# Kernel optimization log

Hardware: AMD Instinct MI355X
Metric: run time of the kernel (lower is better)

The kernel has to match this reference:

```python
import jax, jax.numpy as jnp
import numpy as np

L, D, H, KS, VS, HID = 2048, 1024, 16, 1024, 1024, 4096
EPS = 1e-5


def _linear_params(key, din, dout):
    # torch nn.Linear default init: U(-1/sqrt(din), 1/sqrt(din))
    s = 1.0 / np.sqrt(din)
    kw, kb = jax.random.split(key)
    W = jax.random.uniform(kw, (dout, din), minval=-s, maxval=s, dtype=jnp.float32)
    b = jax.random.uniform(kb, (dout,), minval=-s, maxval=s, dtype=jnp.float32)
    return W, b


def setup_inputs() -> dict:
    key = jax.random.key(0)
    ks = jax.random.split(key, 12)
    x = jax.random.normal(ks[0], (L, D), dtype=jnp.float32)
    # inverse shortest-path lengths in [0, 1]
    shortest_path = jax.random.uniform(ks[1], (L, L), dtype=jnp.float32)
    Wq, bq = _linear_params(ks[2], D, KS)
    Wk, bk = _linear_params(ks[3], D, KS)
    Wv, bv = _linear_params(ks[4], D, VS)
    Wqp, bqp = _linear_params(ks[5], KS, KS)
    Wkp, bkp = _linear_params(ks[6], KS, KS)
    Wvp, bvp = _linear_params(ks[7], VS, VS)
    Wo, bo = _linear_params(ks[8], VS, D)
    W1, b1 = _linear_params(ks[9], D, HID)
    W2, b2 = _linear_params(ks[10], HID, D)
    g1 = jnp.ones((D,), jnp.float32); be1 = jnp.zeros((D,), jnp.float32)
    g2 = jnp.ones((D,), jnp.float32); be2 = jnp.zeros((D,), jnp.float32)
    return dict(x=x, shortest_path=shortest_path,
                Wq=Wq, bq=bq, Wk=Wk, bk=bk, Wv=Wv, bv=bv,
                Wqp=Wqp, bqp=bqp, Wkp=Wkp, bkp=bkp, Wvp=Wvp, bvp=bvp,
                Wo=Wo, bo=bo, W1=W1, b1=b1, W2=W2, b2=b2,
                g1=g1, be1=be1, g2=g2, be2=be2)


def _dense(h, W, b):
    return h @ W.T + b


def _layernorm(h, g, b):
    mu = jnp.mean(h, axis=-1, keepdims=True)
    var = jnp.mean(jnp.square(h - mu), axis=-1, keepdims=True)
    return (h - mu) * jax.lax.rsqrt(var + EPS) * g + b


def reference(x, shortest_path, Wq, bq, Wk, bk, Wv, bv, Wqp, bqp, Wkp, bkp,
              Wvp, bvp, Wo, bo, W1, b1, W2, b2, g1, be1, g2, be2):
    hd = KS // H
    vhd = VS // H
    q = _dense(_dense(x, Wq, bq), Wqp, bqp).reshape(L, H, hd).transpose(1, 0, 2)   # [H,L,hd]
    k = _dense(_dense(x, Wk, bk), Wkp, bkp).reshape(L, H, hd).transpose(1, 0, 2)   # [H,L,hd]
    v = _dense(_dense(x, Wv, bv), Wvp, bvp).reshape(L, H, vhd).transpose(1, 0, 2)  # [H,L,vhd]
    att = jnp.einsum('hld,hmd->hlm', q, k) / jnp.sqrt(jnp.float32(hd))             # [H,L,L]
    sp_bias = jax.nn.softmax(shortest_path, axis=-1) * 0.5                          # [L,L]
    att = jax.nn.softmax(att + sp_bias[None, :, :], axis=-1)
    o = jnp.einsum('hlm,hmd->hld', att, v).transpose(1, 0, 2).reshape(L, VS)        # [L,VS]
    o = _dense(o, Wo, bo)
    h = _layernorm(x + o, g1, be1)                # residual + LN1 (dropout=identity)
    f = jax.nn.relu(_dense(jax.nn.relu(_dense(h, W1, b1)), W2, b2))
    return _layernorm(h + f, g2, be2)             # residual + LN2
```

## Files before the change

kernel.cpp:

```cpp
#include <hip/hip_runtime.h>

typedef __attribute__((ext_vector_type(4))) float f32x4;
typedef __attribute__((ext_vector_type(8))) short s16x8;

static __device__ __forceinline__ ushort f2b(float f) {
  union { float f; unsigned u; } v; v.f = f;
  unsigned u = v.u;
  unsigned r = (u + 0x7fffu + ((u >> 16) & 1u)) >> 16;
  return (ushort)r;
}
static __device__ __forceinline__ float b2f(ushort h) {
  union { unsigned u; float f; } v; v.u = ((unsigned)h) << 16;
  return v.f;
}
static __device__ __forceinline__ unsigned cvtpk(float a, float b) {
  unsigned r;
  asm("v_cvt_pk_bf16_f32 %0, %1, %2" : "=v"(r) : "v"(a), "v"(b));
  return r;
}

static __device__ __forceinline__ void gload_lds16(const ushort* g, ushort* l) {
  __builtin_amdgcn_global_load_lds(
      (const __attribute__((address_space(1))) void*)g,
      (__attribute__((address_space(3))) void*)l, 16, 0, 0);
}

struct Cvt7 {
  const float* src[7];
  ushort* dst[7];
  int n[7];
};
__global__ __launch_bounds__(256) void cvt_multi_k(Cvt7 a) {
  int e = blockIdx.y;
  int i = (blockIdx.x * 256 + threadIdx.x) * 4;
  if (i >= a.n[e]) return;
  float4 v4 = *(const float4*)(a.src[e] + i);
  ushort4 o4; o4.x = f2b(v4.x); o4.y = f2b(v4.y); o4.z = f2b(v4.z); o4.w = f2b(v4.w);
  *(ushort4*)(a.dst[e] + i) = o4;
}

__global__ __launch_bounds__(256) void wtr_k(const float* __restrict__ Wq,
                                             const float* __restrict__ Wk,
                                             const float* __restrict__ Wv,
                                             ushort* __restrict__ dst) {
  __shared__ float t[64][65];
  int z = blockIdx.z;
  const float* src = z == 0 ? Wq : (z == 1 ? Wk : Wv);
  float scale = z == 0 ? 0.125f : 1.f;
  int r0 = blockIdx.x * 64, c0 = blockIdx.y * 64;
  int lr = threadIdx.x >> 2, lc4 = (threadIdx.x & 3) * 16;
#pragma unroll
  for (int j = 0; j < 4; ++j)
    *(float4*)&t[lr][lc4 + j * 4] = *(const float4*)(src + (size_t)(r0 + lr) * 1024 + c0 + lc4 + j * 4);
  __syncthreads();
  ushort tmp[16];
#pragma unroll
  for (int j = 0; j < 16; ++j) tmp[j] = f2b(t[lc4 + j][lr] * scale);
  ushort* d = dst + (size_t)z * 1048576 + (size_t)(c0 + lr) * 1024 + r0 + lc4;
  *(uint4*)d = *(uint4*)tmp;
  *(uint4*)(d + 8) = *(uint4*)(tmp + 8);
}

__global__ __launch_bounds__(256) void bvec_k(
    const float* __restrict__ Wqp, const float* __restrict__ Wkp, const float* __restrict__ Wvp,
    const float* __restrict__ bq, const float* __restrict__ bqp,
    const float* __restrict__ bk, const float* __restrict__ bkp,
    const float* __restrict__ bv, const float* __restrict__ bvp,
    float* __restrict__ outb) {
  int r = blockIdx.x * 4 + (threadIdx.x >> 6);
  int lane = threadIdx.x & 63;
  int z = r >> 10, rr = r & 1023;
  const float* Wp = z == 0 ? Wqp : (z == 1 ? Wkp : Wvp);
  const float* bi = z == 0 ? bq : (z == 1 ? bk : bv);
  const float* bp = z == 0 ? bqp : (z == 1 ? bkp : bvp);
  float s = 0.f;
#pragma unroll
  for (int t = 0; t < 4; ++t) {
    float4 w = *(const float4*)(Wp + (size_t)rr * 1024 + lane * 16 + t * 4);
    float4 b = *(const float4*)(bi + lane * 16 + t * 4);
    s += w.x * b.x + w.y * b.y + w.z * b.z + w.w * b.w;
  }
#pragma unroll
  for (int m = 1; m < 64; m <<= 1) s += __shfl_xor(s, m);
  if (lane == 0) outb[r] = (s + bp[rr]) * (z == 0 ? 0.125f : 1.f);
}

__global__ __launch_bounds__(256) void spsm_k(const float* __restrict__ sp,
                                              ushort* __restrict__ out) {
  const int Lc = 2048;
  int row = blockIdx.x;
  int tid = threadIdx.x;
  const float* r = sp + (size_t)row * Lc;
  float v[8];
  float mx = -1e30f;
#pragma unroll
  for (int j = 0; j < 8; ++j) { v[j] = r[tid + j * 256]; mx = fmaxf(mx, v[j]); }
#pragma unroll
  for (int m = 1; m < 64; m <<= 1) mx = fmaxf(mx, __shfl_xor(mx, m));
  __shared__ float redm[4], reds[4];
  if ((tid & 63) == 0) redm[tid >> 6] = mx;
  __syncthreads();
  mx = fmaxf(fmaxf(redm[0], redm[1]), fmaxf(redm[2], redm[3]));
  float s = 0.f;
#pragma unroll
  for (int j = 0; j < 8; ++j) { v[j] = __expf(v[j] - mx); s += v[j]; }
#pragma unroll
  for (int m = 1; m < 64; m <<= 1) s += __shfl_xor(s, m);
  if ((tid & 63) == 0) reds[tid >> 6] = s;
  __syncthreads();
  s = reds[0] + reds[1] + reds[2] + reds[3];
  float inv = 0.5f / s;
  ushort* o = out + (size_t)row * Lc;
#pragma unroll
  for (int j = 0; j < 8; ++j) o[tid + j * 256] = f2b(v[j] * inv);
}

__global__ __launch_bounds__(256) void vtr_k(const ushort* __restrict__ qkv,
                                             ushort* __restrict__ vT) {
  __shared__ ushort t[64][72];
  int tid = threadIdx.x;
  int r = tid >> 3, c8 = (tid & 7) * 8;
  int l0 = blockIdx.x * 64, h = blockIdx.y;
#pragma unroll
  for (int p = 0; p < 2; ++p)
    *(uint4*)&t[r + p * 32][c8] =
        *(const uint4*)(qkv + (size_t)(l0 + r + p * 32) * 3072 + 2048 + h * 64 + c8);
  __syncthreads();
#pragma unroll
  for (int p = 0; p < 2; ++p) {
    int d = r + p * 32;
    ushort tmp[8];
#pragma unroll
    for (int j = 0; j < 8; ++j) tmp[j] = t[c8 + j][d];
    *(uint4*)(vT + ((size_t)h * 64 + d) * 2048 + l0 + c8) = *(uint4*)tmp;
  }
}

template <int BM, int ZM>
__global__ __launch_bounds__(256, 2) void gemm_k(
    const ushort* __restrict__ A, const ushort* __restrict__ W,
    const float* __restrict__ bias, void* __restrict__ Cv,
    int M, int N, int K, int relu, float oscale) {
  constexpr int MT = BM / 32;
  __shared__ ushort As0[BM][64], Bs0[128][64];
  __shared__ ushort As1[BM][64], Bs1[128][64];
  const int z = (ZM != 0) ? blockIdx.z : 0;
  if (ZM == 1) { A += (size_t)z * M * K; W += (size_t)z * N * K; }
  int kb0 = 0, kb1 = K;
  if (ZM == 2) { int kh = K >> 1; kb0 = z * kh; kb1 = kb0 + kh; }
  const int tid = threadIdx.x;
  const int lane = tid & 63;
  const int wave = tid >> 6;
  const int wm = (wave >> 1) * (BM / 2);
  const int wn = (wave & 1) * 64;
  const int bm = blockIdx.x * BM;
  const int bn = blockIdx.y * 128;
  const int cl = lane & 15, rg = lane >> 4;
  const int lrow = lane >> 3, lcol = (lane & 7) * 8;

  f32x4 acc[MT][4];
#pragma unroll
  for (int i = 0; i < MT; ++i)
#pragma unroll
    for (int j = 0; j < 4; ++j) acc[i][j] = (f32x4){0.f, 0.f, 0.f, 0.f};

  const ushort* gA = A + (size_t)(bm + wave * 8 + lrow) * K + lcol;
  const ushort* gB = W + (size_t)(bn + wave * 8 + lrow) * K + lcol;

  auto stage = [&](ushort* lA, ushort* lB, int k0) {
#pragma unroll
    for (int c = 0; c < MT; ++c)
      gload_lds16(gA + (size_t)(c * 32) * K + k0, lA + wave * 512 + c * 2048);
#pragma unroll
    for (int c = 0; c < 4; ++c)
      gload_lds16(gB + (size_t)(c * 32) * K + k0, lB + wave * 512 + c * 2048);
  };
  auto compute = [&](const ushort* As, const ushort* Bs) {
    const int kbo = 8 * rg;
#pragma unroll
    for (int kk = 0; kk < 64; kk += 32) {
      s16x8 af[MT], bf[4];
#pragma unroll
      for (int mt = 0; mt < MT; ++mt)
        af[mt] = *(const s16x8*)(As + (wm + mt * 16 + cl) * 64 + kk + kbo);
#pragma unroll
      for (int nt = 0; nt < 4; ++nt)
        bf[nt] = *(const s16x8*)(Bs + (wn + nt * 16 + cl) * 64 + kk + kbo);
#pragma unroll
      for (int mt = 0; mt < MT; ++mt)
#pragma unroll
        for (int nt = 0; nt < 4; ++nt)
          acc[mt][nt] = __builtin_amdgcn_mfma_f32_16x16x32_bf16(af[mt], bf[nt], acc[mt][nt], 0, 0, 0);
    }
  };

  const int ktiles = (kb1 - kb0) >> 6;
  stage(&As0[0][0], &Bs0[0][0], kb0);
  __syncthreads();
  for (int tt = 0; tt < ktiles; tt += 2) {
    stage(&As1[0][0], &Bs1[0][0], kb0 + (tt + 1) * 64);
    compute(&As0[0][0], &Bs0[0][0]);
    __syncthreads();
    if (tt + 2 < ktiles) stage(&As0[0][0], &Bs0[0][0], kb0 + (tt + 2) * 64);
    compute(&As1[0][0], &Bs1[0][0]);
    __syncthreads();
  }

  if (ZM == 2) {
    float* Cf = (float*)Cv + (size_t)z * M * N;
#pragma unroll
    for (int nt = 0; nt < 4; ++nt) {
      int c = bn + wn + nt * 16 + cl;
#pragma unroll
      for (int mt = 0; mt < MT; ++mt)
#pragma unroll
        for (int i = 0; i < 4; ++i) {
          int r = bm + wm + mt * 16 + rg * 4 + i;
          Cf[(size_t)r * N + c] = acc[mt][nt][i];
        }
    }
  } else {
    ushort* Cu = (ushort*)Cv;
    if (ZM == 1) Cu += (size_t)z * M * N;
#pragma unroll
    for (int nt = 0; nt < 4; ++nt) {
      int c = bn + wn + nt * 16 + cl;
      float bv = bias ? bias[c] : 0.f;
#pragma unroll
      for (int mt = 0; mt < MT; ++mt) {
        float v0 = (acc[mt][nt][0] + bv) * oscale;
        float v1 = (acc[mt][nt][1] + bv) * oscale;
        float v2 = (acc[mt][nt][2] + bv) * oscale;
        float v3 = (acc[mt][nt][3] + bv) * oscale;
        if (relu) {
          v0 = fmaxf(v0, 0.f); v1 = fmaxf(v1, 0.f);
          v2 = fmaxf(v2, 0.f); v3 = fmaxf(v3, 0.f);
        }
        unsigned p01 = cvtpk(v0, v1), p23 = cvtpk(v2, v3);
        size_t b = (size_t)(bm + wm + mt * 16 + rg * 4) * N + c;
        Cu[b] = (ushort)p01;
        Cu[b + N] = (ushort)(p01 >> 16);
        Cu[b + 2 * N] = (ushort)p23;
        Cu[b + 3 * N] = (ushort)(p23 >> 16);
      }
    }
  }
}

__global__ __launch_bounds__(256, 2) void attn_k(
    const ushort* __restrict__ qkv, const ushort* __restrict__ vT,
    const ushort* __restrict__ biasb, ushort* __restrict__ opart,
    float* __restrict__ lbuf) {
  const int Lc = 2048;
  int h = blockIdx.x;
  int m0 = blockIdx.y * 64;
  int s = blockIdx.z;
  int nb = s * 1024, ne = nb + 1024;
  int tid = threadIdx.x, lane = tid & 63, wave = tid >> 6;

  __shared__ ushort Ks[64][72];
  __shared__ ushort Vs[64][72];
  __shared__ ushort Ps[4][16][72];
  __shared__ ushort Bs2[64][72];

  const int rg = lane >> 4, cl = lane & 15;
  const int kb = 8 * rg;
  int srow = tid >> 3, scol = (tid & 7) * 8;

  const ushort* qp = qkv + (size_t)(m0 + wave * 16 + cl) * 3072 + h * 64;
  s16x8 qfr[2];
  qfr[0] = *(const s16x8*)(qp + kb);
  qfr[1] = *(const s16x8*)(qp + 32 + kb);

  f32x4 oacc[4];
#pragma unroll
  for (int i = 0; i < 4; ++i) oacc[i] = (f32x4){0.f, 0.f, 0.f, 0.f};
  float lacc[4] = {0.f, 0.f, 0.f, 0.f};

  for (int n0 = nb; n0 < ne; n0 += 64) {
    __syncthreads();
#pragma unroll
    for (int pp = 0; pp < 2; ++pp) {
      int r = srow + pp * 32;
      *(uint4*)&Ks[r][scol] = *(const uint4*)(qkv + (size_t)(n0 + r) * 3072 + 1024 + h * 64 + scol);
      *(uint4*)&Vs[r][scol] = *(const uint4*)(vT + ((size_t)h * 64 + r) * 2048 + n0 + scol);
      *(uint4*)&Bs2[r][scol] = *(const uint4*)(biasb + (size_t)(m0 + r) * Lc + n0 + scol);
    }
    __syncthreads();

    f32x4 sacc[4];
#pragma unroll
    for (int nt = 0; nt < 4; ++nt)
#pragma unroll
      for (int i = 0; i < 4; ++i)
        sacc[nt][i] = b2f(Bs2[wave * 16 + rg * 4 + i][nt * 16 + cl]) - 8.f;

    __builtin_amdgcn_s_setprio(1);
#pragma unroll
    for (int kk2 = 0; kk2 < 2; ++kk2) {
#pragma unroll
      for (int nt = 0; nt < 4; ++nt) {
        s16x8 b = *(const s16x8*)&Ks[nt * 16 + cl][kk2 * 32 + kb];
        sacc[nt] = __builtin_amdgcn_mfma_f32_16x16x32_bf16(qfr[kk2], b, sacc[nt], 0, 0, 0);
      }
    }
    __builtin_amdgcn_s_setprio(0);

#pragma unroll
    for (int i = 0; i < 4; ++i) {
#pragma unroll
      for (int nt = 0; nt < 4; ++nt) {
        float pv = __expf(sacc[nt][i]);
        sacc[nt][i] = pv;
        lacc[i] += pv;
      }
    }
#pragma unroll
    for (int nt = 0; nt < 4; ++nt) {
      unsigned p01 = cvtpk(sacc[nt][0], sacc[nt][1]);
      unsigned p23 = cvtpk(sacc[nt][2], sacc[nt][3]);
      Ps[wave][rg * 4 + 0][nt * 16 + cl] = (ushort)p01;
      Ps[wave][rg * 4 + 1][nt * 16 + cl] = (ushort)(p01 >> 16);
      Ps[wave][rg * 4 + 2][nt * 16 + cl] = (ushort)p23;
      Ps[wave][rg * 4 + 3][nt * 16 + cl] = (ushort)(p23 >> 16);
    }
    __builtin_amdgcn_s_setprio(1);
#pragma unroll
    for (int kk = 0; kk < 64; kk += 32) {
      s16x8 a = *(const s16x8*)&Ps[wave][cl][kk + kb];
#pragma unroll
      for (int nt = 0; nt < 4; ++nt) {
        s16x8 b = *(const s16x8*)&Vs[nt * 16 + cl][kk + kb];
        oacc[nt] = __builtin_amdgcn_mfma_f32_16x16x32_bf16(a, b, oacc[nt], 0, 0, 0);
      }
    }
    __builtin_amdgcn_s_setprio(0);
  }
#pragma unroll
  for (int nt = 0; nt < 4; ++nt) {
    unsigned p01 = cvtpk(oacc[nt][0], oacc[nt][1]);
    unsigned p23 = cvtpk(oacc[nt][2], oacc[nt][3]);
    size_t b = ((size_t)s * Lc + (m0 + wave * 16 + rg * 4)) * 1024 + h * 64 + nt * 16 + cl;
    opart[b] = (ushort)p01;
    opart[b + 1024] = (ushort)(p01 >> 16);
    opart[b + 2048] = (ushort)p23;
    opart[b + 3072] = (ushort)(p23 >> 16);
  }
#pragma unroll
  for (int i = 0; i < 4; ++i) {
    float l = lacc[i];
#pragma unroll
    for (int m = 1; m < 16; m <<= 1) l += __shfl_xor(l, m);
    if (cl == 0) {
      int r = m0 + wave * 16 + rg * 4 + i;
      lbuf[(size_t)(s * 16 + h) * Lc + r] = l;
    }
  }
}

__global__ __launch_bounds__(256) void acomb_k(const ushort* __restrict__ op,
                                               const float* __restrict__ lbuf,
                                               ushort* __restrict__ ob) {
  const int Lc = 2048;
  int qrow = blockIdx.x;
  int tid = threadIdx.x;
  int c = tid * 4;
  int h = c >> 6;
  float l0 = lbuf[(size_t)h * Lc + qrow];
  float l1 = lbuf[(size_t)(16 + h) * Lc + qrow];
  float inv = 1.f / (l0 + l1);
  ushort4 a = *(const ushort4*)(op + (size_t)qrow * 1024 + c);
  ushort4 b = *(const ushort4*)(op + ((size_t)Lc + qrow) * 1024 + c);
  ushort4 o;
  o.x = f2b((b2f(a.x) + b2f(b.x)) * inv);
  o.y = f2b((b2f(a.y) + b2f(b.y)) * inv);
  o.z = f2b((b2f(a.z) + b2f(b.z)) * inv);
  o.w = f2b((b2f(a.w) + b2f(b.w)) * inv);
  *(ushort4*)(ob + (size_t)qrow * 1024 + c) = o;
}

__global__ __launch_bounds__(256) void lnf_k(const float* __restrict__ basef,
                                             const float* __restrict__ p,
                                             const float* __restrict__ bvec,
                                             const float* __restrict__ g,
                                             const float* __restrict__ be,
                                             int relu,
                                             ushort* __restrict__ outb,
                                             float* __restrict__ outf) {
  const int Dc = 1024;
  const size_t MN = (size_t)2048 * 1024;
  int row = blockIdx.x;
  int tid = threadIdx.x;
  int c = tid * 4;
  float4 bx = *(const float4*)(basef + (size_t)row * Dc + c);
  float4 a0 = *(const float4*)(p + (size_t)row * Dc + c);
  float4 a1 = *(const float4*)(p + MN + (size_t)row * Dc + c);
  float4 bb = *(const float4*)(bvec + c);
  float v0 = a0.x + a1.x + bb.x, v1 = a0.y + a1.y + bb.y;
  float v2 = a0.z + a1.z + bb.z, v3 = a0.w + a1.w + bb.w;
  if (relu) {
    v0 = fmaxf(v0, 0.f); v1 = fmaxf(v1, 0.f);
    v2 = fmaxf(v2, 0.f); v3 = fmaxf(v3, 0.f);
  }
  v0 += bx.x; v1 += bx.y; v2 += bx.z; v3 += bx.w;
  float s = v0 + v1 + v2 + v3;
  __shared__ float red[4];
#pragma unroll
  for (int m = 1; m < 64; m <<= 1) s += __shfl_xor(s, m);
  if ((tid & 63) == 0) red[tid >> 6] = s;
  __syncthreads();
  s = red[0] + red[1] + red[2] + red[3];
  float mu = s * (1.f / Dc);
  float d0 = v0 - mu, d1 = v1 - mu, d2 = v2 - mu, d3 = v3 - mu;
  float ss = d0 * d0 + d1 * d1 + d2 * d2 + d3 * d3;
  __syncthreads();
#pragma unroll
  for (int m = 1; m < 64; m <<= 1) ss += __shfl_xor(ss, m);
  if ((tid & 63) == 0) red[tid >> 6] = ss;
  __syncthreads();
  ss = red[0] + red[1] + red[2] + red[3];
  float rs = rsqrtf(ss * (1.f / Dc) + 1e-5f);
  float4 gv = *(const float4*)(g + c);
  float4 bev = *(const float4*)(be + c);
  float y0 = d0 * rs * gv.x + bev.x;
  float y1 = d1 * rs * gv.y + bev.y;
  float y2 = d2 * rs * gv.z + bev.z;
  float y3 = d3 * rs * gv.w + bev.w;
  size_t o = (size_t)row * Dc + c;
  if (outb) {
    ushort4 ob4; ob4.x = f2b(y0); ob4.y = f2b(y1); ob4.z = f2b(y2); ob4.w = f2b(y3);
    *(ushort4*)(outb + o) = ob4;
  }
  if (outf) {
    float4 of4; of4.x = y0; of4.y = y1; of4.z = y2; of4.w = y3;
    *(float4*)(outf + o) = of4;
  }
}

extern "C" void kernel_launch(void* const* d_in, const int* in_sizes, int n_in,
                              void* d_out, int out_size, void* d_ws, size_t ws_size,
                              hipStream_t stream) {
  const int L = 2048, D = 1024, H = 16, HID = 4096;
  const float* x   = (const float*)d_in[0];
  const float* sp  = (const float*)d_in[1];
  const float* Wq  = (const float*)d_in[2];  const float* bq  = (const float*)d_in[3];
  const float* Wk  = (const float*)d_in[4];  const float* bk  = (const float*)d_in[5];
  const float* Wv  = (const float*)d_in[6];  const float* bv  = (const float*)d_in[7];
  const float* Wqp = (const float*)d_in[8];  const float* bqp = (const float*)d_in[9];
  const float* Wkp = (const float*)d_in[10]; const float* bkp = (const float*)d_in[11];
  const float* Wvp = (const float*)d_in[12]; const float* bvp = (const float*)d_in[13];
  const float* Wo  = (const float*)d_in[14]; const float* bo  = (const float*)d_in[15];
  const float* W1  = (const float*)d_in[16]; const float* b1  = (const float*)d_in[17];
  const float* W2  = (const float*)d_in[18]; const float* b2  = (const float*)d_in[19];
  const float* g1  = (const float*)d_in[20]; const float* be1 = (const float*)d_in[21];
  const float* g2  = (const float*)d_in[22]; const float* be2 = (const float*)d_in[23];
  float* out = (float*)d_out;

  size_t off = 0;
  char* base = (char*)d_ws;
  auto alloc = [&](size_t b) {
    char* p = base + off;
    off += (b + 255) & ~(size_t)255;
    return p;
  };
  ushort* xb    = (ushort*)alloc((size_t)L * D * 2);
  ushort* wqpb  = (ushort*)alloc((size_t)D * D * 2);
  ushort* wkpb  = (ushort*)alloc((size_t)D * D * 2);
  ushort* wvpb  = (ushort*)alloc((size_t)D * D * 2);
  ushort* wqTb  = (ushort*)alloc((size_t)3 * D * D * 2);
  ushort* wfused= (ushort*)alloc((size_t)3 * D * D * 2);
  ushort* qkv   = (ushort*)alloc((size_t)L * 3072 * 2);
  float*  bfused= (float*)alloc((size_t)3072 * 4);
  ushort* wob   = (ushort*)alloc((size_t)D * D * 2);
  ushort* w1b   = (ushort*)alloc((size_t)HID * D * 2);
  ushort* w2b   = (ushort*)alloc((size_t)D * HID * 2);
  ushort* spsb  = (ushort*)alloc((size_t)L * L * 2);
  ushort* opart = (ushort*)alloc((size_t)2 * L * 1024 * 2);
  ushort* vT    = (ushort*)alloc((size_t)H * 64 * L * 2);
  float*  lbuf  = (float*)alloc((size_t)2 * H * L * 4);
  ushort* ob    = (ushort*)alloc((size_t)L * 1024 * 2);
  ushort* hb    = (ushort*)alloc((size_t)L * D * 2);
  float*  hf    = (float*)alloc((size_t)L * D * 4);

  ushort* ffn1  = wqTb;
  float*  parts = (float*)spsb;

  Cvt7 ca;
  ca.src[0] = x;   ca.dst[0] = xb;   ca.n[0] = L * D;
  ca.src[1] = Wqp; ca.dst[1] = wqpb; ca.n[1] = D * D;
  ca.src[2] = Wkp; ca.dst[2] = wkpb; ca.n[2] = D * D;
  ca.src[3] = Wvp; ca.dst[3] = wvpb; ca.n[3] = D * D;
  ca.src[4] = Wo;  ca.dst[4] = wob;  ca.n[4] = D * D;
  ca.src[5] = W1;  ca.dst[5] = w1b;  ca.n[5] = HID * D;
  ca.src[6] = W2;  ca.dst[6] = w2b;  ca.n[6] = D * HID;
  cvt_multi_k<<<dim3(4096, 7), dim3(256), 0, stream>>>(ca);

  wtr_k<<<dim3(16, 16, 3), dim3(256), 0, stream>>>(Wq, Wk, Wv, wqTb);
  bvec_k<<<dim3(768), dim3(256), 0, stream>>>(Wqp, Wkp, Wvp, bq, bqp, bk, bkp, bv, bvp, bfused);
  spsm_k<<<dim3(L), dim3(256), 0, stream>>>(sp, spsb);

  gemm_k<64, 1><<<dim3(16, 8, 3), dim3(256), 0, stream>>>(
      wqpb, wqTb, (const float*)nullptr, wfused, D, D, D, 0, 1.f);
  gemm_k<64, 0><<<dim3(32, 24), dim3(256), 0, stream>>>(
      xb, wfused, bfused, qkv, L, 3072, D, 0, 1.f);

  vtr_k<<<dim3(L / 64, H), dim3(256), 0, stream>>>(qkv, vT);
  attn_k<<<dim3(H, L / 64, 2), dim3(256), 0, stream>>>(qkv, vT, spsb, opart, lbuf);
  acomb_k<<<dim3(L), dim3(256), 0, stream>>>(opart, lbuf, ob);

  gemm_k<64, 2><<<dim3(32, 8, 2), dim3(256), 0, stream>>>(
      ob, wob, (const float*)nullptr, parts, L, D, D, 0, 1.f);
  lnf_k<<<dim3(L), dim3(256), 0, stream>>>(x, parts, bo, g1, be1, 0, hb, hf);
  gemm_k<128, 0><<<dim3(16, 32), dim3(256), 0, stream>>>(
      hb, w1b, b1, ffn1, L, HID, D, 1, 1.f);
  gemm_k<64, 2><<<dim3(32, 8, 2), dim3(256), 0, stream>>>(
      ffn1, w2b, (const float*)nullptr, parts, L, D, HID, 0, 1.f);
  lnf_k<<<dim3(L), dim3(256), 0, stream>>>(hf, parts, b2, g2, be2, 1, (ushort*)nullptr, out);
}
```

Measured before the change: 218.7 us.

## Drop split-KV attention; double-buffer K/V/bias tiles and normalize in-kernel

The attention kernel no longer splits the key range into two halves and no longer needs a separate combine kernel. Each block now walks all 2048 keys and prefetches the next K, V and bias tile into registers, then into a second LDS buffer, while it computes on the current one. It normalizes by the row sum before writing the bf16 output, which removes the partial-output and l-buffer traffic and one launch. The cost is half as many attention blocks (512) and more LDS per block, which may lower occupancy. BM=64 GEMMs also get a launch-bounds hint of 3 blocks per CU.

```diff
diff --git a/kernel.cpp b/kernel.cpp
--- a/kernel.cpp
+++ b/kernel.cpp
@@ -137,7 +137,7 @@
 }
 
 template <int BM, int ZM>
-__global__ __launch_bounds__(256, 2) void gemm_k(
+__global__ __launch_bounds__(256, BM == 64 ? 3 : 2) void gemm_k(
     const ushort* __restrict__ A, const ushort* __restrict__ W,
     const float* __restrict__ bias, void* __restrict__ Cv,
     int M, int N, int K, int relu, float oscale) {
@@ -249,60 +249,87 @@
 
 __global__ __launch_bounds__(256, 2) void attn_k(
     const ushort* __restrict__ qkv, const ushort* __restrict__ vT,
-    const ushort* __restrict__ biasb, ushort* __restrict__ opart,
-    float* __restrict__ lbuf) {
+    const ushort* __restrict__ biasb, ushort* __restrict__ ob) {
   const int Lc = 2048;
   int h = blockIdx.x;
   int m0 = blockIdx.y * 64;
-  int s = blockIdx.z;
-  int nb = s * 1024, ne = nb + 1024;
   int tid = threadIdx.x, lane = tid & 63, wave = tid >> 6;
 
-  __shared__ ushort Ks[64][72];
-  __shared__ ushort Vs[64][72];
+  __shared__ ushort KsA[64][72], VsA[64][72], BsA[64][72];
+  __shared__ ushort KsB[64][72], VsB[64][72], BsB[64][72];
   __shared__ ushort Ps[4][16][72];
-  __shared__ ushort Bs2[64][72];
 
   const int rg = lane >> 4, cl = lane & 15;
   const int kb = 8 * rg;
   int srow = tid >> 3, scol = (tid & 7) * 8;
 
   const ushort* qp = qkv + (size_t)(m0 + wave * 16 + cl) * 3072 + h * 64;
-  s16x8 qfr[2];
-  qfr[0] = *(const s16x8*)(qp + kb);
-  qfr[1] = *(const s16x8*)(qp + 32 + kb);
+  s16x8 qfr0 = *(const s16x8*)(qp + kb);
+  s16x8 qfr1 = *(const s16x8*)(qp + 32 + kb);
+
+  const ushort* kbase0 = qkv + (size_t)srow * 3072 + 1024 + h * 64 + scol;
+  const ushort* kbase1 = qkv + (size_t)(srow + 32) * 3072 + 1024 + h * 64 + scol;
+  const ushort* vbase0 = vT + ((size_t)h * 64 + srow) * 2048 + scol;
+  const ushort* vbase1 = vT + ((size_t)h * 64 + srow + 32) * 2048 + scol;
+  const ushort* bbase0 = biasb + (size_t)(m0 + srow) * Lc + scol;
+  const ushort* bbase1 = biasb + (size_t)(m0 + srow + 32) * Lc + scol;
 
   f32x4 oacc[4];
 #pragma unroll
   for (int i = 0; i < 4; ++i) oacc[i] = (f32x4){0.f, 0.f, 0.f, 0.f};
   float lacc[4] = {0.f, 0.f, 0.f, 0.f};
 
-  for (int n0 = nb; n0 < ne; n0 += 64) {
-    __syncthreads();
-#pragma unroll
-    for (int pp = 0; pp < 2; ++pp) {
-      int r = srow + pp * 32;
-      *(uint4*)&Ks[r][scol] = *(const uint4*)(qkv + (size_t)(n0 + r) * 3072 + 1024 + h * 64 + scol);
-      *(uint4*)&Vs[r][scol] = *(const uint4*)(vT + ((size_t)h * 64 + r) * 2048 + n0 + scol);
-      *(uint4*)&Bs2[r][scol] = *(const uint4*)(biasb + (size_t)(m0 + r) * Lc + n0 + scol);
-    }
-    __syncthreads();
+  uint4 kr0, kr1, vr0, vr1, br0, br1;
+  auto LOAD = [&](int n0) {
+    kr0 = *(const uint4*)(kbase0 + (size_t)n0 * 3072);
+    kr1 = *(const uint4*)(kbase1 + (size_t)n0 * 3072);
+    vr0 = *(const uint4*)(vbase0 + n0);
+    vr1 = *(const uint4*)(vbase1 + n0);
+    br0 = *(const uint4*)(bbase0 + n0);
+    br1 = *(const uint4*)(bbase1 + n0);
+  };
+  auto STORE = [&](ushort (*Kc)[72], ushort (*Vc)[72], ushort (*Bc)[72]) {
+    *(uint4*)&Kc[srow][scol] = kr0;
+    *(uint4*)&Kc[srow + 32][scol] = kr1;
+    *(uint4*)&Vc[srow][scol] = vr0;
+    *(uint4*)&Vc[srow + 32][scol] = vr1;
+    *(uint4*)&Bc[srow][scol] = br0;
+    *(uint4*)&Bc[srow + 32][scol] = br1;
+  };
+
+  LOAD(0);
+  STORE(KsA, VsA, BsA);
+  __syncthreads();
+
+  for (int n0 = 0; n0 < Lc; n0 += 64) {
+    bool odd = (n0 >> 6) & 1;
+    ushort(*Kc)[72] = odd ? KsB : KsA;
+    ushort(*Vc)[72] = odd ? VsB : VsA;
+    ushort(*Bc)[72] = odd ? BsB : BsA;
+    ushort(*Kn)[72] = odd ? KsA : KsB;
+    ushort(*Vn)[72] = odd ? VsA : VsB;
+    ushort(*Bn)[72] = odd ? BsA : BsB;
+
+    bool more = (n0 + 64) < Lc;
+    if (more) LOAD(n0 + 64);
 
     f32x4 sacc[4];
 #pragma unroll
     for (int nt = 0; nt < 4; ++nt)
 #pragma unroll
       for (int i = 0; i < 4; ++i)
-        sacc[nt][i] = b2f(Bs2[wave * 16 + rg * 4 + i][nt * 16 + cl]) - 8.f;
+        sacc[nt][i] = b2f(Bc[wave * 16 + rg * 4 + i][nt * 16 + cl]) - 8.f;
 
     __builtin_amdgcn_s_setprio(1);
 #pragma unroll
-    for (int kk2 = 0; kk2 < 2; ++kk2) {
-#pragma unroll
-      for (int nt = 0; nt < 4; ++nt) {
-        s16x8 b = *(const s16x8*)&Ks[nt * 16 + cl][kk2 * 32 + kb];
-        sacc[nt] = __builtin_amdgcn_mfma_f32_16x16x32_bf16(qfr[kk2], b, sacc[nt], 0, 0, 0);
-      }
+    for (int nt = 0; nt < 4; ++nt) {
+      s16x8 b = *(const s16x8*)&Kc[nt * 16 + cl][kb];
+      sacc[nt] = __builtin_amdgcn_mfma_f32_16x16x32_bf16(qfr0, b, sacc[nt], 0, 0, 0);
+    }
+#pragma unroll
+    for (int nt = 0; nt < 4; ++nt) {
+      s16x8 b = *(const s16x8*)&Kc[nt * 16 + cl][32 + kb];
+      sacc[nt] = __builtin_amdgcn_mfma_f32_16x16x32_bf16(qfr1, b, sacc[nt], 0, 0, 0);
     }
     __builtin_amdgcn_s_setprio(0);
 
@@ -330,53 +357,34 @@
       s16x8 a = *(const s16x8*)&Ps[wave][cl][kk + kb];
 #pragma unroll
       for (int nt = 0; nt < 4; ++nt) {
-        s16x8 b = *(const s16x8*)&Vs[nt * 16 + cl][kk + kb];
+        s16x8 b = *(const s16x8*)&Vc[nt * 16 + cl][kk + kb];
         oacc[nt] = __builtin_amdgcn_mfma_f32_16x16x32_bf16(a, b, oacc[nt], 0, 0, 0);
       }
     }
     __builtin_amdgcn_s_setprio(0);
-  }
-#pragma unroll
-  for (int nt = 0; nt < 4; ++nt) {
-    unsigned p01 = cvtpk(oacc[nt][0], oacc[nt][1]);
-    unsigned p23 = cvtpk(oacc[nt][2], oacc[nt][3]);
-    size_t b = ((size_t)s * Lc + (m0 + wave * 16 + rg * 4)) * 1024 + h * 64 + nt * 16 + cl;
-    opart[b] = (ushort)p01;
-    opart[b + 1024] = (ushort)(p01 >> 16);
-    opart[b + 2048] = (ushort)p23;
-    opart[b + 3072] = (ushort)(p23 >> 16);
-  }
+
+    if (more) STORE(Kn, Vn, Bn);
+    __syncthreads();
+  }
+
+  float linv[4];
 #pragma unroll
   for (int i = 0; i < 4; ++i) {
     float l = lacc[i];
 #pragma unroll
     for (int m = 1; m < 16; m <<= 1) l += __shfl_xor(l, m);
-    if (cl == 0) {
-      int r = m0 + wave * 16 + rg * 4 + i;
-      lbuf[(size_t)(s * 16 + h) * Lc + r] = l;
-    }
-  }
-}
-
-__global__ __launch_bounds__(256) void acomb_k(const ushort* __restrict__ op,
-                                               const float* __restrict__ lbuf,
-                                               ushort* __restrict__ ob) {
-  const int Lc = 2048;
-  int qrow = blockIdx.x;
-  int tid = threadIdx.x;
-  int c = tid * 4;
-  int h = c >> 6;
-  float l0 = lbuf[(size_t)h * Lc + qrow];
-  float l1 = lbuf[(size_t)(16 + h) * Lc + qrow];
-  float inv = 1.f / (l0 + l1);
-  ushort4 a = *(const ushort4*)(op + (size_t)qrow * 1024 + c);
-  ushort4 b = *(const ushort4*)(op + ((size_t)Lc + qrow) * 1024 + c);
-  ushort4 o;
-  o.x = f2b((b2f(a.x) + b2f(b.x)) * inv);
-  o.y = f2b((b2f(a.y) + b2f(b.y)) * inv);
-  o.z = f2b((b2f(a.z) + b2f(b.z)) * inv);
-  o.w = f2b((b2f(a.w) + b2f(b.w)) * inv);
-  *(ushort4*)(ob + (size_t)qrow * 1024 + c) = o;
+    linv[i] = 1.f / l;
+  }
+#pragma unroll
+  for (int nt = 0; nt < 4; ++nt) {
+    unsigned p01 = cvtpk(oacc[nt][0] * linv[0], oacc[nt][1] * linv[1]);
+    unsigned p23 = cvtpk(oacc[nt][2] * linv[2], oacc[nt][3] * linv[3]);
+    size_t b = (size_t)(m0 + wave * 16 + rg * 4) * 1024 + h * 64 + nt * 16 + cl;
+    ob[b] = (ushort)p01;
+    ob[b + 1024] = (ushort)(p01 >> 16);
+    ob[b + 2048] = (ushort)p23;
+    ob[b + 3072] = (ushort)(p23 >> 16);
+  }
 }
 
 __global__ __launch_bounds__(256) void lnf_k(const float* __restrict__ basef,
@@ -475,12 +483,12 @@
   ushort* w1b   = (ushort*)alloc((size_t)HID * D * 2);
   ushort* w2b   = (ushort*)alloc((size_t)D * HID * 2);
   ushort* spsb  = (ushort*)alloc((size_t)L * L * 2);
-  ushort* opart = (ushort*)alloc((size_t)2 * L * 1024 * 2);
+  ushort* extra = (ushort*)alloc((size_t)2 * L * 1024 * 2);
   ushort* vT    = (ushort*)alloc((size_t)H * 64 * L * 2);
-  float*  lbuf  = (float*)alloc((size_t)2 * H * L * 4);
   ushort* ob    = (ushort*)alloc((size_t)L * 1024 * 2);
   ushort* hb    = (ushort*)alloc((size_t)L * D * 2);
   float*  hf    = (float*)alloc((size_t)L * D * 4);
+  (void)extra;
 
   ushort* ffn1  = wqTb;
   float*  parts = (float*)spsb;
@@ -505,8 +513,7 @@
       xb, wfused, bfused, qkv, L, 3072, D, 0, 1.f);
 
   vtr_k<<<dim3(L / 64, H), dim3(256), 0, stream>>>(qkv, vT);
-  attn_k<<<dim3(H, L / 64, 2), dim3(256), 0, stream>>>(qkv, vT, spsb, opart, lbuf);
-  acomb_k<<<dim3(L), dim3(256), 0, stream>>>(opart, lbuf, ob);
+  attn_k<<<dim3(H, L / 64), dim3(256), 0, stream>>>(qkv, vT, spsb, ob);
 
   gemm_k<64, 2><<<dim3(32, 8, 2), dim3(256), 0, stream>>>(
       ob, wob, (const float*)nullptr, parts, L, D, D, 0, 1.f);
```

After: 217.9 us. No clear change (-0.4%).

## Pre-permute softmax bias to MFMA fragment layout and use exp2 in attention

Applied to the files above, without the earlier changes.

Folds log2(e) into the Q projection scale and bias so attention can use the raw v_exp_f32 (exp2) in place of __expf. The shortest-path softmax bias is written in a layout that matches the MFMA accumulator fragments, so each lane reads its bias values straight from global memory. This drops the Bs2 shared-memory tile and the LDS staging traffic and frees LDS for higher occupancy, and the launch bounds are raised for attention and BM=64 GEMMs. The risks are register pressure from the higher occupancy targets, and bias reads that are now strided 2-byte global loads rather than coalesced vector loads.

```diff
diff --git a/kernel.cpp b/kernel.cpp
--- a/kernel.cpp
+++ b/kernel.cpp
@@ -18,12 +18,19 @@
   asm("v_cvt_pk_bf16_f32 %0, %1, %2" : "=v"(r) : "v"(a), "v"(b));
   return r;
 }
+static __device__ __forceinline__ float exp2i(float x) {
+  float r;
+  asm("v_exp_f32 %0, %1" : "=v"(r) : "v"(x));
+  return r;
+}
 
 static __device__ __forceinline__ void gload_lds16(const ushort* g, ushort* l) {
   __builtin_amdgcn_global_load_lds(
       (const __attribute__((address_space(1))) void*)g,
       (__attribute__((address_space(3))) void*)l, 16, 0, 0);
 }
+
+#define LOG2E 1.44269504f
 
 struct Cvt7 {
   const float* src[7];
@@ -46,7 +53,7 @@
   __shared__ float t[64][65];
   int z = blockIdx.z;
   const float* src = z == 0 ? Wq : (z == 1 ? Wk : Wv);
-  float scale = z == 0 ? 0.125f : 1.f;
+  float scale = z == 0 ? 0.125f * LOG2E : 1.f;
   int r0 = blockIdx.x * 64, c0 = blockIdx.y * 64;
   int lr = threadIdx.x >> 2, lc4 = (threadIdx.x & 3) * 16;
 #pragma unroll
@@ -82,11 +89,11 @@
   }
 #pragma unroll
   for (int m = 1; m < 64; m <<= 1) s += __shfl_xor(s, m);
-  if (lane == 0) outb[r] = (s + bp[rr]) * (z == 0 ? 0.125f : 1.f);
+  if (lane == 0) outb[r] = (s + bp[rr]) * (z == 0 ? 0.125f * LOG2E : 1.f);
 }
 
 __global__ __launch_bounds__(256) void spsm_k(const float* __restrict__ sp,
-                                              ushort* __restrict__ out) {
+                                              ushort* __restrict__ outP) {
   const int Lc = 2048;
   int row = blockIdx.x;
   int tid = threadIdx.x;
@@ -109,10 +116,16 @@
   if ((tid & 63) == 0) reds[tid >> 6] = s;
   __syncthreads();
   s = reds[0] + reds[1] + reds[2] + reds[3];
-  float inv = 0.5f / s;
-  ushort* o = out + (size_t)row * Lc;
-#pragma unroll
-  for (int j = 0; j < 8; ++j) o[tid + j * 256] = f2b(v[j] * inv);
+  float inv = 0.5f * LOG2E / s;
+  int mb = row >> 6, rr = row & 63;
+  int wv = rr >> 4, rem = rr & 15, rg = rem >> 2, ii = rem & 3;
+  size_t rbase = ((size_t)mb * 32) * 4096 + (size_t)wv * 1024 + (size_t)ii * 256 + (size_t)rg * 16;
+#pragma unroll
+  for (int j = 0; j < 8; ++j) {
+    int col = tid + j * 256;
+    int nb = col >> 6, cc = col & 63, nt = cc >> 4, cl = cc & 15;
+    outP[rbase + (size_t)nb * 4096 + nt * 64 + cl] = f2b(v[j] * inv);
+  }
 }
 
 __global__ __launch_bounds__(256) void vtr_k(const ushort* __restrict__ qkv,
@@ -137,7 +150,7 @@
 }
 
 template <int BM, int ZM>
-__global__ __launch_bounds__(256, 2) void gemm_k(
+__global__ __launch_bounds__(256, BM == 64 ? 3 : 2) void gemm_k(
     const ushort* __restrict__ A, const ushort* __restrict__ W,
     const float* __restrict__ bias, void* __restrict__ Cv,
     int M, int N, int K, int relu, float oscale) {
@@ -247,9 +260,9 @@
   }
 }
 
-__global__ __launch_bounds__(256, 2) void attn_k(
+__global__ __launch_bounds__(256, 4) void attn_k(
     const ushort* __restrict__ qkv, const ushort* __restrict__ vT,
-    const ushort* __restrict__ biasb, ushort* __restrict__ opart,
+    const ushort* __restrict__ biasP, ushort* __restrict__ opart,
     float* __restrict__ lbuf) {
   const int Lc = 2048;
   int h = blockIdx.x;
@@ -261,16 +274,16 @@
   __shared__ ushort Ks[64][72];
   __shared__ ushort Vs[64][72];
   __shared__ ushort Ps[4][16][72];
-  __shared__ ushort Bs2[64][72];
 
   const int rg = lane >> 4, cl = lane & 15;
   const int kb = 8 * rg;
   int srow = tid >> 3, scol = (tid & 7) * 8;
 
   const ushort* qp = qkv + (size_t)(m0 + wave * 16 + cl) * 3072 + h * 64;
-  s16x8 qfr[2];
-  qfr[0] = *(const s16x8*)(qp + kb);
-  qfr[1] = *(const s16x8*)(qp + 32 + kb);
+  s16x8 qfr0 = *(const s16x8*)(qp + kb);
+  s16x8 qfr1 = *(const s16x8*)(qp + 32 + kb);
+
+  const ushort* bpB = biasP + ((size_t)(m0 >> 6) * 32) * 4096 + (size_t)wave * 1024 + lane;
 
   f32x4 oacc[4];
 #pragma unroll
@@ -284,33 +297,35 @@
       int r = srow + pp * 32;
       *(uint4*)&Ks[r][scol] = *(const uint4*)(qkv + (size_t)(n0 + r) * 3072 + 1024 + h * 64 + scol);
       *(uint4*)&Vs[r][scol] = *(const uint4*)(vT + ((size_t)h * 64 + r) * 2048 + n0 + scol);
-      *(uint4*)&Bs2[r][scol] = *(const uint4*)(biasb + (size_t)(m0 + r) * Lc + n0 + scol);
     }
     __syncthreads();
 
+    const ushort* bp = bpB + (size_t)(n0 >> 6) * 4096;
     f32x4 sacc[4];
 #pragma unroll
-    for (int nt = 0; nt < 4; ++nt)
-#pragma unroll
-      for (int i = 0; i < 4; ++i)
-        sacc[nt][i] = b2f(Bs2[wave * 16 + rg * 4 + i][nt * 16 + cl]) - 8.f;
+    for (int i = 0; i < 4; ++i)
+#pragma unroll
+      for (int nt = 0; nt < 4; ++nt)
+        sacc[nt][i] = b2f(bp[(i * 4 + nt) * 64]) - 8.f * LOG2E;
 
     __builtin_amdgcn_s_setprio(1);
 #pragma unroll
-    for (int kk2 = 0; kk2 < 2; ++kk2) {
+    for (int nt = 0; nt < 4; ++nt) {
+      s16x8 b = *(const s16x8*)&Ks[nt * 16 + cl][kb];
+      sacc[nt] = __builtin_amdgcn_mfma_f32_16x16x32_bf16(qfr0, b, sacc[nt], 0, 0, 0);
+    }
+#pragma unroll
+    for (int nt = 0; nt < 4; ++nt) {
+      s16x8 b = *(const s16x8*)&Ks[nt * 16 + cl][32 + kb];
+      sacc[nt] = __builtin_amdgcn_mfma_f32_16x16x32_bf16(qfr1, b, sacc[nt], 0, 0, 0);
+    }
+    __builtin_amdgcn_s_setprio(0);
+
+#pragma unroll
+    for (int i = 0; i < 4; ++i) {
 #pragma unroll
       for (int nt = 0; nt < 4; ++nt) {
-        s16x8 b = *(const s16x8*)&Ks[nt * 16 + cl][kk2 * 32 + kb];
-        sacc[nt] = __builtin_amdgcn_mfma_f32_16x16x32_bf16(qfr[kk2], b, sacc[nt], 0, 0, 0);
-      }
-    }
-    __builtin_amdgcn_s_setprio(0);
-
-#pragma unroll
-    for (int i = 0; i < 4; ++i) {
-#pragma unroll
-      for (int nt = 0; nt < 4; ++nt) {
-        float pv = __expf(sacc[nt][i]);
+        float pv = exp2i(sacc[nt][i]);
         sacc[nt][i] = pv;
         lacc[i] += pv;
       }
```

New measurement: 215.7 us. About the same (-1.4%).
